# Kernel optimization log

Hardware: AMD Instinct MI355X
Metric: run time of the kernel (lower is better)

Reference implementation:

```python
import jax, jax.numpy as jnp
import numpy as np

B, NQ, NK = 4, 2048, 2048
CQ, CK = 1024, 768
H = 16
D = CQ // H  # 64
EPS = 1e-5


def layernorm(x, gamma, beta):
    mu = jnp.mean(x, axis=-1, keepdims=True)
    var = jnp.var(x, axis=-1, keepdims=True)
    return (x - mu) * jax.lax.rsqrt(var + EPS) * gamma + beta


def setup_inputs() -> dict:
    key = jax.random.key(0)
    ks = jax.random.split(key, 12)
    s_q = 1.0 / np.sqrt(CQ)
    s_c = 1.0 / np.sqrt(CK)
    return {
        "query_tokens": jax.random.normal(ks[0], (B, NQ, CQ), jnp.float32),
        "context_tokens": jax.random.normal(ks[1], (B, NK, CK), jnp.float32),
        "Wq": jax.random.uniform(ks[2], (CQ, CQ), jnp.float32, -s_q, s_q),
        "bq": jnp.zeros((CQ,), jnp.float32),
        "Wk": jax.random.uniform(ks[3], (CK, CQ), jnp.float32, -s_c, s_c),
        "bk": jnp.zeros((CQ,), jnp.float32),
        "Wv": jax.random.uniform(ks[4], (CK, CQ), jnp.float32, -s_c, s_c),
        "bv": jnp.zeros((CQ,), jnp.float32),
        "Wo": jax.random.uniform(ks[5], (CQ, CQ), jnp.float32, -s_q, s_q),
        "bo": jnp.zeros((CQ,), jnp.float32),
        "gamma_q": jnp.ones((CQ,), jnp.float32),
        "beta_q": jnp.zeros((CQ,), jnp.float32),
        "gamma_ctx": jnp.ones((CK,), jnp.float32),
        "beta_ctx": jnp.zeros((CK,), jnp.float32),
    }


def reference(query_tokens, context_tokens, Wq, bq, Wk, bk, Wv, bv, Wo, bo,
              gamma_q, beta_q, gamma_ctx, beta_ctx):
    scale = 1.0 / np.sqrt(D)
    xq = layernorm(query_tokens, gamma_q, beta_q)      # [B,NQ,CQ]
    xc = layernorm(context_tokens, gamma_ctx, beta_ctx)  # [B,NK,CK]
    q = (xq @ Wq + bq).reshape(B, NQ, H, D)
    k = (xc @ Wk + bk).reshape(B, NK, H, D)
    v = (xc @ Wv + bv).reshape(B, NK, H, D)
    scores = jnp.einsum('bqhd,bkhd->bhqk', q, k) * scale  # [B,H,NQ,NK]
    attn = jax.nn.softmax(scores, axis=-1)
    attended = jnp.einsum('bhqk,bkhd->bqhd', attn, v).reshape(B, NQ, CQ)
    return attended @ Wo + bo
```

## Files before the change

kernel.cpp:

```cpp
#include <hip/hip_runtime.h>
#include <hip/hip_bf16.h>
#include <stdint.h>

#define B_    4
#define NQ_   2048
#define NK_   2048
#define CQ_   1024
#define CK_   768
#define H_    16
#define D_    64
#define SCALE 0.125f
#define C2    0.1803368801111204f

typedef __attribute__((ext_vector_type(8))) short bf16x8;
typedef __attribute__((ext_vector_type(4))) float f32x4;
typedef __attribute__((ext_vector_type(4))) unsigned int u32x4;

#define MFMA16(a, b, c) __builtin_amdgcn_mfma_f32_16x16x32_bf16((a), (b), (c), 0, 0, 0)

#define GLL16(gp, lp)                                                                 \
    __builtin_amdgcn_global_load_lds(                                                 \
        (__attribute__((address_space(1))) uint32_t*)(uintptr_t)(gp),                 \
        (__attribute__((address_space(3))) uint32_t*)(uintptr_t)(lp), 16, 0, 0)

__device__ inline unsigned short f2bf(float f) {
    union { float f; uint32_t u; } v; v.f = f;
    uint32_t u = v.u;
    return (unsigned short)((u + 0x7fffu + ((u >> 16) & 1u)) >> 16);
}

__device__ inline uint32_t packbf2(float a, float b) {
    union { __hip_bfloat162 h; uint32_t u; } v;
    v.h = __float22bfloat162_rn(float2{a, b});
    return v.u;
}

__global__ __launch_bounds__(256) void ln_fused(const float* __restrict__ xqt,
                                                const float* __restrict__ xct,
                                                const float* __restrict__ gq,
                                                const float* __restrict__ btq,
                                                const float* __restrict__ gc,
                                                const float* __restrict__ btc,
                                                unsigned short* __restrict__ oq,
                                                unsigned short* __restrict__ oc) {
    int row = blockIdx.x;
    const float *x, *gamma, *beta;
    unsigned short* out;
    int W;
    float invW;
    if (row < 8192) {
        x = xqt + (size_t)row * 1024; gamma = gq; beta = btq;
        out = oq + (size_t)row * 1024; W = 1024; invW = 1.f / 1024.f;
    } else {
        int r = row - 8192;
        x = xct + (size_t)r * 768; gamma = gc; beta = btc;
        out = oc + (size_t)r * 768; W = 768; invW = 1.f / 768.f;
    }
    int tid = threadIdx.x;
    int col = tid * 4;
    float v0 = 0.f, v1 = 0.f, v2 = 0.f, v3 = 0.f;
    float s = 0.f, s2 = 0.f;
    bool active = (col < W);
    if (active) {
        float4 vv = *(const float4*)(x + col);
        v0 = vv.x; v1 = vv.y; v2 = vv.z; v3 = vv.w;
        s = v0 + v1 + v2 + v3;
        s2 = v0 * v0 + v1 * v1 + v2 * v2 + v3 * v3;
    }
    for (int off = 32; off >= 1; off >>= 1) {
        s += __shfl_xor(s, off);
        s2 += __shfl_xor(s2, off);
    }
    __shared__ float red[8];
    __shared__ float stat[2];
    int wid = tid >> 6, lane = tid & 63;
    if (lane == 0) { red[wid] = s; red[4 + wid] = s2; }
    __syncthreads();
    if (tid == 0) {
        float ts = red[0] + red[1] + red[2] + red[3];
        float ts2 = red[4] + red[5] + red[6] + red[7];
        float mu = ts * invW;
        float var = ts2 * invW - mu * mu;
        stat[0] = mu;
        stat[1] = rsqrtf(var + 1e-5f);
    }
    __syncthreads();
    float mu = stat[0], rstd = stat[1];
    if (active) {
        float4 g = *(const float4*)(gamma + col);
        float4 b = *(const float4*)(beta + col);
        ushort4 o;
        o.x = f2bf((v0 - mu) * rstd * g.x + b.x);
        o.y = f2bf((v1 - mu) * rstd * g.y + b.y);
        o.z = f2bf((v2 - mu) * rstd * g.z + b.z);
        o.w = f2bf((v3 - mu) * rstd * g.w + b.w);
        *(ushort4*)(out + col) = o;
    }
}

__global__ __launch_bounds__(256) void transpose_all(const float* __restrict__ Wq,
                                                     const float* __restrict__ Wk,
                                                     const float* __restrict__ Wv,
                                                     const float* __restrict__ Wo,
                                                     unsigned short* __restrict__ Wqt,
                                                     unsigned short* __restrict__ Wkvt,
                                                     unsigned short* __restrict__ Wot) {
    __shared__ float t[32][33];
    int blk = blockIdx.x;
    const float* src;
    unsigned short* dst;
    int K;
    if (blk < 1024)      { src = Wq; dst = Wqt; K = 1024; }
    else if (blk < 1792) { blk -= 1024; src = Wk; dst = Wkvt; K = 768; }
    else if (blk < 2560) { blk -= 1792; src = Wv; dst = Wkvt + (size_t)1024 * 768; K = 768; }
    else                 { blk -= 2560; src = Wo; dst = Wot; K = 1024; }
    int n0 = (blk & 31) * 32, k0 = (blk >> 5) * 32;
    int tx = threadIdx.x, ty = threadIdx.y;
    for (int i = 0; i < 4; i++)
        t[ty + 8 * i][tx] = src[(size_t)(k0 + ty + 8 * i) * 1024 + n0 + tx];
    __syncthreads();
    for (int i = 0; i < 4; i++)
        dst[(size_t)(n0 + ty + 8 * i) * K + k0 + tx] = f2bf(t[tx][ty + 8 * i]);
}

template <int MODE>
__global__ __launch_bounds__(256) void gemm_bt(const unsigned short* __restrict__ X,
                                               const unsigned short* __restrict__ Wt,
                                               const float* __restrict__ bias0,
                                               const float* __restrict__ bias1,
                                               void* __restrict__ out0,
                                               void* __restrict__ out1, int Kd) {
    constexpr int NB = (MODE == 3) ? 16 : 8;
    __shared__ __align__(16) unsigned short As[128 * 64];
    __shared__ __align__(16) unsigned short Bs[128 * 64];
    int tid = threadIdx.x;
    int lane = tid & 63, wid = tid >> 6;

    int lin = blockIdx.y * NB + blockIdx.x;
    int virt = (lin & 7) * (NB * 8) + (lin >> 3);
    int m0 = (virt / NB) * 128;
    int n0 = (virt % NB) * 128;
    int wm = wid >> 1, wn = wid & 1;

    f32x4 acc[4][4];
    for (int i = 0; i < 4; i++)
        for (int j = 0; j < 4; j++) acc[i][j] = (f32x4){0.f, 0.f, 0.f, 0.f};

    int srow = wid * 8 + (lane >> 3);
    int sxor = ((lane & 7) * 16) ^ (((lane >> 3) & 7) << 4);
    int swz = (lane & 7) << 4;
    const char* Xb = (const char*)X;
    const char* Wb = (const char*)Wt;
    char* AsB = (char*)As;
    char* BsB = (char*)Bs;

    for (int k0 = 0; k0 < Kd; k0 += 64) {
        for (int i = 0; i < 4; i++) {
            int row = i * 32 + srow;
            GLL16(Xb + ((size_t)(m0 + row) * Kd + k0) * 2 + sxor, AsB + i * 4096 + wid * 1024);
            GLL16(Wb + ((size_t)(n0 + row) * Kd + k0) * 2 + sxor, BsB + i * 4096 + wid * 1024);
        }
        __syncthreads();
        for (int kk = 0; kk < 2; kk++) {
            int cb = (((lane >> 4) * 16 + kk * 64) ^ swz);
            bf16x8 a[4], b[4];
            for (int mf = 0; mf < 4; mf++)
                a[mf] = *(const bf16x8*)(AsB + (wm * 64 + mf * 16 + (lane & 15)) * 128 + cb);
            for (int nf = 0; nf < 4; nf++)
                b[nf] = *(const bf16x8*)(BsB + (wn * 64 + nf * 16 + (lane & 15)) * 128 + cb);
            for (int mf = 0; mf < 4; mf++)
                for (int nf = 0; nf < 4; nf++) acc[mf][nf] = MFMA16(a[mf], b[nf], acc[mf][nf]);
        }
        __syncthreads();
    }

    int crow0 = m0 + wm * 64;
    int ccol0 = n0 + wn * 64;
    for (int nf = 0; nf < 4; nf++) {
        int col = ccol0 + nf * 16 + (lane & 15);
        float bv_;
        if (MODE == 3)
            bv_ = (col < 1024) ? bias0[col] : bias1[col - 1024];
        else
            bv_ = bias0[col];
        for (int mf = 0; mf < 4; mf++) {
            int rowb = crow0 + mf * 16 + (lane >> 4) * 4;
            for (int r = 0; r < 4; r++) {
                int row = rowb + r;
                float val = acc[mf][nf][r] + bv_;
                if (MODE == 2) {
                    ((float*)out0)[(size_t)row * 1024 + col] = val;
                } else {
                    int b = row >> 11, nq = row & 2047;
                    unsigned short bfv = f2bf(val);
                    if (MODE == 0) {
                        int h = col >> 6, d = col & 63;
                        ((unsigned short*)out0)[(((size_t)(b * H_ + h)) * NQ_ + nq) * 64 + d] = bfv;
                    } else {
                        if (col < 1024) {
                            int h = col >> 6, d = col & 63;
                            ((unsigned short*)out0)[(((size_t)(b * H_ + h)) * NQ_ + nq) * 64 + d] = bfv;
                        } else {
                            int c = col - 1024;
                            int h = c >> 6, d = c & 63;
                            int u = nq & 63;
                            int p = (u & 32) + ((u & 12) << 1) + ((u & 16) >> 2) + (u & 3);
                            int nq_p = (nq & ~63) | p;
                            ((unsigned short*)out1)[(((size_t)(b * H_ + h)) * 64 + d) * NK_ + nq_p] = bfv;
                        }
                    }
                }
            }
        }
    }
}

__global__ __launch_bounds__(512, 4) void flash_attn(const unsigned short* __restrict__ Q,
                                                     const unsigned short* __restrict__ K,
                                                     const unsigned short* __restrict__ Vt,
                                                     unsigned short* __restrict__ attended) {
    __shared__ __align__(16) char smem[2][16384];
    int tid = threadIdx.x, lane = tid & 63, wid = tid >> 6;
    int g = lane >> 4;
    int q = lane & 15;

    const f32x4 zero4 = {0.f, 0.f, 0.f, 0.f};

    int lin = blockIdx.y * 8 + blockIdx.x;
    int virt = (lin & 7) * 64 + (lin >> 3);
    int bh = virt >> 3;
    int q0 = (virt & 7) * 256;
    const char* Qb = (const char*)(Q + (size_t)bh * NQ_ * 64);
    const char* Kb = (const char*)(K + (size_t)bh * NK_ * 64);
    const char* Vb = (const char*)(Vt + (size_t)bh * 64 * NK_);

    int qrow = q0 + wid * 32 + q;
    bf16x8 qf0[2], qf1[2];
    qf0[0] = *(const bf16x8*)(Qb + (size_t)qrow * 128 + g * 16);
    qf0[1] = *(const bf16x8*)(Qb + (size_t)qrow * 128 + g * 16 + 64);
    qf1[0] = *(const bf16x8*)(Qb + (size_t)(qrow + 16) * 128 + g * 16);
    qf1[1] = *(const bf16x8*)(Qb + (size_t)(qrow + 16) * 128 + g * 16 + 64);

    bf16x8 onesf;
#pragma unroll
    for (int i = 0; i < 8; i++) onesf[i] = (short)0x3f80;

    f32x4 acc0[4], acc1[4];
    for (int i = 0; i < 4; i++) {
        acc0[i] = zero4;
        acc1[i] = zero4;
    }
    f32x4 accl0 = zero4, accl1 = zero4;
    float mst = -3.0e38f;

    int sxor = ((lane & 7) * 16) ^ (((lane >> 3) & 7) << 4);
    const char* kptr = Kb + (size_t)(wid * 8 + (lane >> 3)) * 128 + sxor;
    const char* vptr = Vb + (size_t)(wid * 8 + (lane >> 3)) * 4096 + sxor;
    int cb0 = g * 16;
    int swz = (lane & 7) << 4;

    GLL16(kptr, smem[0] + wid * 1024);
    GLL16(vptr, smem[0] + 8192 + wid * 1024);
    kptr += 8192;
    vptr += 128;
    __syncthreads();
    int cur = 0;

    for (int t = 0; t < NK_ / 64; ++t) {
        if (t < NK_ / 64 - 1) {
            GLL16(kptr, smem[cur ^ 1] + wid * 1024);
            GLL16(vptr, smem[cur ^ 1] + 8192 + wid * 1024);
            kptr += 8192;
            vptr += 128;
        }
        const char* Ksb = smem[cur];
        const char* Vsb = smem[cur] + 8192;

        f32x4 s0[4], s1[4];
        __builtin_amdgcn_s_setprio(1);
#pragma unroll
        for (int nf = 0; nf < 4; nf++) {
            bf16x8 kf0 = *(const bf16x8*)(Ksb + (nf * 16 + q) * 128 + (cb0 ^ swz));
            bf16x8 kf1 = *(const bf16x8*)(Ksb + (nf * 16 + q) * 128 + ((cb0 + 64) ^ swz));
            s0[nf] = MFMA16(kf0, qf0[0], zero4);
            s0[nf] = MFMA16(kf1, qf0[1], s0[nf]);
            s1[nf] = MFMA16(kf0, qf1[0], zero4);
            s1[nf] = MFMA16(kf1, qf1[1], s1[nf]);
        }
        __builtin_amdgcn_s_setprio(0);

#define VMAX4(a, b) (f32x4){fmaxf(a[0], b[0]), fmaxf(a[1], b[1]), fmaxf(a[2], b[2]), fmaxf(a[3], b[3])}
        f32x4 x0 = VMAX4(s0[0], s1[0]);
        f32x4 x1 = VMAX4(s0[1], s1[1]);
        f32x4 x2 = VMAX4(s0[2], s1[2]);
        f32x4 x3 = VMAX4(s0[3], s1[3]);
        x0 = VMAX4(x0, x2);
        x1 = VMAX4(x1, x3);
        x0 = VMAX4(x0, x1);
        float mloc = fmaxf(fmaxf(x0[0], x0[1]), fmaxf(x0[2], x0[3]));
        mloc = fmaxf(mloc, __shfl_xor(mloc, 16));
        mloc = fmaxf(mloc, __shfl_xor(mloc, 32));

        if (!__all(mloc - mst <= 44.36f)) {
            float mnew = fmaxf(mst, mloc);
            float alpha = __builtin_amdgcn_exp2f((mst - mnew) * C2);
            mst = mnew;
            float al[4];
#pragma unroll
            for (int r = 0; r < 4; r++) al[r] = __shfl(alpha, 4 * g + r);
#pragma unroll
            for (int r = 0; r < 4; r++) {
#pragma unroll
                for (int df = 0; df < 4; df++) {
                    acc0[df][r] *= al[r];
                    acc1[df][r] *= al[r];
                }
                accl0[r] *= al[r];
                accl1[r] *= al[r];
            }
        }
        float mc = mst * C2;

        __builtin_amdgcn_s_setprio(1);
#pragma unroll
        for (int kk = 0; kk < 2; kk++) {
            float p0v[8], p1v[8];
#pragma unroll
            for (int h = 0; h < 2; h++)
#pragma unroll
                for (int r = 0; r < 4; r++) {
                    p0v[4 * h + r] = __builtin_amdgcn_exp2f(s0[2 * kk + h][r] * C2 - mc);
                    p1v[4 * h + r] = __builtin_amdgcn_exp2f(s1[2 * kk + h][r] * C2 - mc);
                }
            union { u32x4 u; bf16x8 b; } ap0, ap1;
            ap0.u[0] = packbf2(p0v[0], p0v[1]);
            ap0.u[1] = packbf2(p0v[2], p0v[3]);
            ap0.u[2] = packbf2(p0v[4], p0v[5]);
            ap0.u[3] = packbf2(p0v[6], p0v[7]);
            ap1.u[0] = packbf2(p1v[0], p1v[1]);
            ap1.u[1] = packbf2(p1v[2], p1v[3]);
            ap1.u[2] = packbf2(p1v[4], p1v[5]);
            ap1.u[3] = packbf2(p1v[6], p1v[7]);

            accl0 = MFMA16(ap0.b, onesf, accl0);
            accl1 = MFMA16(ap1.b, onesf, accl1);
#pragma unroll
            for (int df = 0; df < 4; df++) {
                bf16x8 bv = *(const bf16x8*)(Vsb + (df * 16 + q) * 128 + ((cb0 + kk * 64) ^ swz));
                acc0[df] = MFMA16(ap0.b, bv, acc0[df]);
                acc1[df] = MFMA16(ap1.b, bv, acc1[df]);
            }
        }
        __builtin_amdgcn_s_setprio(0);

        __syncthreads();
        cur ^= 1;
    }

    int b = bh >> 4, h = bh & 15;
#pragma unroll
    for (int df = 0; df < 4; df++)
#pragma unroll
        for (int r = 0; r < 4; r++) {
            int row = q0 + wid * 32 + 4 * g + r;
            int col = h * 64 + df * 16 + q;
            attended[(size_t)(b * NQ_ + row) * CQ_ + col] = f2bf(acc0[df][r] / accl0[r]);
            attended[(size_t)(b * NQ_ + row + 16) * CQ_ + col] = f2bf(acc1[df][r] / accl1[r]);
        }
}

extern "C" void kernel_launch(void* const* d_in, const int* in_sizes, int n_in,
                              void* d_out, int out_size, void* d_ws, size_t ws_size,
                              hipStream_t stream) {
    const float* qt  = (const float*)d_in[0];
    const float* ct  = (const float*)d_in[1];
    const float* Wq  = (const float*)d_in[2];
    const float* bq  = (const float*)d_in[3];
    const float* Wk  = (const float*)d_in[4];
    const float* bk  = (const float*)d_in[5];
    const float* Wv  = (const float*)d_in[6];
    const float* bv  = (const float*)d_in[7];
    const float* Wo  = (const float*)d_in[8];
    const float* bo  = (const float*)d_in[9];
    const float* gq  = (const float*)d_in[10];
    const float* btq = (const float*)d_in[11];
    const float* gc  = (const float*)d_in[12];
    const float* btc = (const float*)d_in[13];

    char* ws = (char*)d_ws;
    unsigned short* xq   = (unsigned short*)(ws + 0);
    unsigned short* xc   = (unsigned short*)(ws + 16777216);
    unsigned short* Wqt  = (unsigned short*)(ws + 29360128);
    unsigned short* Wkvt = (unsigned short*)(ws + 31457280);
    unsigned short* Wot  = (unsigned short*)(ws + 34603008);
    unsigned short* Qb   = (unsigned short*)(ws + 36700160);
    unsigned short* Kb   = (unsigned short*)(ws + 53477376);
    unsigned short* Vtb  = (unsigned short*)(ws + 70254592);

    ln_fused<<<16384, 256, 0, stream>>>(qt, ct, gq, btq, gc, btc, xq, xc);
    transpose_all<<<3584, dim3(32, 8), 0, stream>>>(Wq, Wk, Wv, Wo, Wqt, Wkvt, Wot);

    gemm_bt<0><<<dim3(8, 64), 256, 0, stream>>>(xq, Wqt, bq, nullptr, Qb, nullptr, 1024);
    gemm_bt<3><<<dim3(16, 64), 256, 0, stream>>>(xc, Wkvt, bk, bv, Kb, Vtb, 768);

    flash_attn<<<dim3(8, 64), 512, 0, stream>>>(Qb, Kb, Vtb, xq);

    gemm_bt<2><<<dim3(8, 64), 256, 0, stream>>>(xq, Wot, bo, nullptr, d_out, nullptr, 1024);
}
```

Before: 209.4 us.

## Merge layernorm and weight transpose launches; deepen flash-attn K/V prefetch to four buffers

Merges the layernorm and weight-transpose kernels into a single launch that splits work by block index, removing one kernel launch and its tail. In flash attention, the K/V shared-memory ring grows from two to four 16KB buffers. Two tiles are now processed per barrier and the next two are prefetched after it, so each iteration has one barrier instead of two and loads are issued further ahead. The cost is 64KB of LDS per block, which can lower occupancy below the four blocks per CU that the launch bounds request.

```diff
diff --git a/kernel.cpp b/kernel.cpp
--- a/kernel.cpp
+++ b/kernel.cpp
@@ -35,92 +35,94 @@
     return v.u;
 }
 
-__global__ __launch_bounds__(256) void ln_fused(const float* __restrict__ xqt,
-                                                const float* __restrict__ xct,
-                                                const float* __restrict__ gq,
-                                                const float* __restrict__ btq,
-                                                const float* __restrict__ gc,
-                                                const float* __restrict__ btc,
-                                                unsigned short* __restrict__ oq,
-                                                unsigned short* __restrict__ oc) {
-    int row = blockIdx.x;
-    const float *x, *gamma, *beta;
-    unsigned short* out;
-    int W;
-    float invW;
-    if (row < 8192) {
-        x = xqt + (size_t)row * 1024; gamma = gq; beta = btq;
-        out = oq + (size_t)row * 1024; W = 1024; invW = 1.f / 1024.f;
-    } else {
-        int r = row - 8192;
-        x = xct + (size_t)r * 768; gamma = gc; beta = btc;
-        out = oc + (size_t)r * 768; W = 768; invW = 1.f / 768.f;
-    }
-    int tid = threadIdx.x;
-    int col = tid * 4;
-    float v0 = 0.f, v1 = 0.f, v2 = 0.f, v3 = 0.f;
-    float s = 0.f, s2 = 0.f;
-    bool active = (col < W);
-    if (active) {
-        float4 vv = *(const float4*)(x + col);
-        v0 = vv.x; v1 = vv.y; v2 = vv.z; v3 = vv.w;
-        s = v0 + v1 + v2 + v3;
-        s2 = v0 * v0 + v1 * v1 + v2 * v2 + v3 * v3;
-    }
-    for (int off = 32; off >= 1; off >>= 1) {
-        s += __shfl_xor(s, off);
-        s2 += __shfl_xor(s2, off);
-    }
+__global__ __launch_bounds__(256) void ln_tr(const float* __restrict__ xqt,
+                                             const float* __restrict__ xct,
+                                             const float* __restrict__ gq,
+                                             const float* __restrict__ btq,
+                                             const float* __restrict__ gc,
+                                             const float* __restrict__ btc,
+                                             unsigned short* __restrict__ oq,
+                                             unsigned short* __restrict__ oc,
+                                             const float* __restrict__ Wq,
+                                             const float* __restrict__ Wk,
+                                             const float* __restrict__ Wv,
+                                             const float* __restrict__ Wo,
+                                             unsigned short* __restrict__ Wqt,
+                                             unsigned short* __restrict__ Wkvt,
+                                             unsigned short* __restrict__ Wot) {
     __shared__ float red[8];
     __shared__ float stat[2];
-    int wid = tid >> 6, lane = tid & 63;
-    if (lane == 0) { red[wid] = s; red[4 + wid] = s2; }
-    __syncthreads();
-    if (tid == 0) {
-        float ts = red[0] + red[1] + red[2] + red[3];
-        float ts2 = red[4] + red[5] + red[6] + red[7];
-        float mu = ts * invW;
-        float var = ts2 * invW - mu * mu;
-        stat[0] = mu;
-        stat[1] = rsqrtf(var + 1e-5f);
-    }
-    __syncthreads();
-    float mu = stat[0], rstd = stat[1];
-    if (active) {
-        float4 g = *(const float4*)(gamma + col);
-        float4 b = *(const float4*)(beta + col);
-        ushort4 o;
-        o.x = f2bf((v0 - mu) * rstd * g.x + b.x);
-        o.y = f2bf((v1 - mu) * rstd * g.y + b.y);
-        o.z = f2bf((v2 - mu) * rstd * g.z + b.z);
-        o.w = f2bf((v3 - mu) * rstd * g.w + b.w);
-        *(ushort4*)(out + col) = o;
-    }
-}
-
-__global__ __launch_bounds__(256) void transpose_all(const float* __restrict__ Wq,
-                                                     const float* __restrict__ Wk,
-                                                     const float* __restrict__ Wv,
-                                                     const float* __restrict__ Wo,
-                                                     unsigned short* __restrict__ Wqt,
-                                                     unsigned short* __restrict__ Wkvt,
-                                                     unsigned short* __restrict__ Wot) {
-    __shared__ float t[32][33];
+    __shared__ float tt[32][33];
     int blk = blockIdx.x;
-    const float* src;
-    unsigned short* dst;
-    int K;
-    if (blk < 1024)      { src = Wq; dst = Wqt; K = 1024; }
-    else if (blk < 1792) { blk -= 1024; src = Wk; dst = Wkvt; K = 768; }
-    else if (blk < 2560) { blk -= 1792; src = Wv; dst = Wkvt + (size_t)1024 * 768; K = 768; }
-    else                 { blk -= 2560; src = Wo; dst = Wot; K = 1024; }
-    int n0 = (blk & 31) * 32, k0 = (blk >> 5) * 32;
-    int tx = threadIdx.x, ty = threadIdx.y;
-    for (int i = 0; i < 4; i++)
-        t[ty + 8 * i][tx] = src[(size_t)(k0 + ty + 8 * i) * 1024 + n0 + tx];
-    __syncthreads();
-    for (int i = 0; i < 4; i++)
-        dst[(size_t)(n0 + ty + 8 * i) * K + k0 + tx] = f2bf(t[tx][ty + 8 * i]);
+    int tid = threadIdx.x;
+
+    if (blk < 16384) {
+        const float *x, *gamma, *beta;
+        unsigned short* out;
+        int W;
+        float invW;
+        if (blk < 8192) {
+            x = xqt + (size_t)blk * 1024; gamma = gq; beta = btq;
+            out = oq + (size_t)blk * 1024; W = 1024; invW = 1.f / 1024.f;
+        } else {
+            int r = blk - 8192;
+            x = xct + (size_t)r * 768; gamma = gc; beta = btc;
+            out = oc + (size_t)r * 768; W = 768; invW = 1.f / 768.f;
+        }
+        int col = tid * 4;
+        float v0 = 0.f, v1 = 0.f, v2 = 0.f, v3 = 0.f;
+        float s = 0.f, s2 = 0.f;
+        bool active = (col < W);
+        if (active) {
+            float4 vv = *(const float4*)(x + col);
+            v0 = vv.x; v1 = vv.y; v2 = vv.z; v3 = vv.w;
+            s = v0 + v1 + v2 + v3;
+            s2 = v0 * v0 + v1 * v1 + v2 * v2 + v3 * v3;
+        }
+        for (int off = 32; off >= 1; off >>= 1) {
+            s += __shfl_xor(s, off);
+            s2 += __shfl_xor(s2, off);
+        }
+        int wid = tid >> 6, lane = tid & 63;
+        if (lane == 0) { red[wid] = s; red[4 + wid] = s2; }
+        __syncthreads();
+        if (tid == 0) {
+            float ts = red[0] + red[1] + red[2] + red[3];
+            float ts2 = red[4] + red[5] + red[6] + red[7];
+            float mu = ts * invW;
+            float var = ts2 * invW - mu * mu;
+            stat[0] = mu;
+            stat[1] = rsqrtf(var + 1e-5f);
+        }
+        __syncthreads();
+        float mu = stat[0], rstd = stat[1];
+        if (active) {
+            float4 gm = *(const float4*)(gamma + col);
+            float4 bt = *(const float4*)(beta + col);
+            ushort4 o;
+            o.x = f2bf((v0 - mu) * rstd * gm.x + bt.x);
+            o.y = f2bf((v1 - mu) * rstd * gm.y + bt.y);
+            o.z = f2bf((v2 - mu) * rstd * gm.z + bt.z);
+            o.w = f2bf((v3 - mu) * rstd * gm.w + bt.w);
+            *(ushort4*)(out + col) = o;
+        }
+    } else {
+        int b2 = blk - 16384;
+        const float* src;
+        unsigned short* dst;
+        int K;
+        if (b2 < 1024)      { src = Wq; dst = Wqt; K = 1024; }
+        else if (b2 < 1792) { b2 -= 1024; src = Wk; dst = Wkvt; K = 768; }
+        else if (b2 < 2560) { b2 -= 1792; src = Wv; dst = Wkvt + (size_t)1024 * 768; K = 768; }
+        else                 { b2 -= 2560; src = Wo; dst = Wot; K = 1024; }
+        int n0 = (b2 & 31) * 32, k0 = (b2 >> 5) * 32;
+        int tx = tid & 31, ty = tid >> 5;
+        for (int i = 0; i < 4; i++)
+            tt[ty + 8 * i][tx] = src[(size_t)(k0 + ty + 8 * i) * 1024 + n0 + tx];
+        __syncthreads();
+        for (int i = 0; i < 4; i++)
+            dst[(size_t)(n0 + ty + 8 * i) * K + k0 + tx] = f2bf(tt[tx][ty + 8 * i]);
+    }
 }
 
 template <int MODE>
@@ -219,7 +221,7 @@
                                                      const unsigned short* __restrict__ K,
                                                      const unsigned short* __restrict__ Vt,
                                                      unsigned short* __restrict__ attended) {
-    __shared__ __align__(16) char smem[2][16384];
+    __shared__ __align__(16) char smem[4][16384];
     int tid = threadIdx.x, lane = tid & 63, wid = tid >> 6;
     int g = lane >> 4;
     int q = lane & 15;
@@ -259,23 +261,7 @@
     int cb0 = g * 16;
     int swz = (lane & 7) << 4;
 
-    GLL16(kptr, smem[0] + wid * 1024);
-    GLL16(vptr, smem[0] + 8192 + wid * 1024);
-    kptr += 8192;
-    vptr += 128;
-    __syncthreads();
-    int cur = 0;
-
-    for (int t = 0; t < NK_ / 64; ++t) {
-        if (t < NK_ / 64 - 1) {
-            GLL16(kptr, smem[cur ^ 1] + wid * 1024);
-            GLL16(vptr, smem[cur ^ 1] + 8192 + wid * 1024);
-            kptr += 8192;
-            vptr += 128;
-        }
-        const char* Ksb = smem[cur];
-        const char* Vsb = smem[cur] + 8192;
-
+    auto TILE = [&](const char* Ksb, const char* Vsb) {
         f32x4 s0[4], s1[4];
         __builtin_amdgcn_s_setprio(1);
 #pragma unroll
@@ -352,9 +338,34 @@
             }
         }
         __builtin_amdgcn_s_setprio(0);
-
-        __syncthreads();
-        cur ^= 1;
+    };
+
+#pragma unroll
+    for (int j = 0; j < 4; j++) {
+        GLL16(kptr, smem[j] + wid * 1024);
+        GLL16(vptr, smem[j] + 8192 + wid * 1024);
+        kptr += 8192;
+        vptr += 128;
+    }
+    __syncthreads();
+
+    for (int i = 0; i < 16; ++i) {
+        int t = 2 * i;
+        const char* B0 = smem[t & 3];
+        const char* B1 = smem[(t + 1) & 3];
+        TILE(B0, B0 + 8192);
+        TILE(B1, B1 + 8192);
+        __syncthreads();
+        if (t + 4 < 32) {
+            GLL16(kptr, smem[t & 3] + wid * 1024);
+            GLL16(vptr, smem[t & 3] + 8192 + wid * 1024);
+            kptr += 8192;
+            vptr += 128;
+            GLL16(kptr, smem[(t + 1) & 3] + wid * 1024);
+            GLL16(vptr, smem[(t + 1) & 3] + 8192 + wid * 1024);
+            kptr += 8192;
+            vptr += 128;
+        }
     }
 
     int b = bh >> 4, h = bh & 15;
@@ -397,8 +408,8 @@
     unsigned short* Kb   = (unsigned short*)(ws + 53477376);
     unsigned short* Vtb  = (unsigned short*)(ws + 70254592);
 
-    ln_fused<<<16384, 256, 0, stream>>>(qt, ct, gq, btq, gc, btc, xq, xc);
-    transpose_all<<<3584, dim3(32, 8), 0, stream>>>(Wq, Wk, Wv, Wo, Wqt, Wkvt, Wot);
+    ln_tr<<<19968, 256, 0, stream>>>(qt, ct, gq, btq, gc, btc, xq, xc,
+                                     Wq, Wk, Wv, Wo, Wqt, Wkvt, Wot);
 
     gemm_bt<0><<<dim3(8, 64), 256, 0, stream>>>(xq, Wqt, bq, nullptr, Qb, nullptr, 1024);
     gemm_bt<3><<<dim3(16, 64), 256, 0, stream>>>(xc, Wkvt, bk, bv, Kb, Vtb, 768);
```

Result: no change. 206.2 us (-1.5%).
